# Kernel tuning notes

Hardware: AMD Instinct MI355X
Metric: run time of the kernel (lower is better)

## Reference

```python
import jax, jax.numpy as jnp
import numpy as np

N, M = 4096, 8192
IN_DIM, OUT_DIM = 4096, 1024
NUM_SAMPLE = 10


def setup_inputs() -> dict:
    key = jax.random.key(0)
    k1, k2, k3, k4, k5 = jax.random.split(key, 5)
    node_features = jax.random.normal(k1, (N, IN_DIM), dtype=jnp.float32)
    neighbor_features = jax.random.normal(k2, (M, IN_DIM), dtype=jnp.float32)
    # Xavier-ish scale for params
    weight = jax.random.normal(k3, (OUT_DIM, IN_DIM), dtype=jnp.float32) * (1.0 / np.sqrt(IN_DIM))
    attention_vector = jax.random.normal(k4, (2 * OUT_DIM, 1), dtype=jnp.float32) * 0.05
    neighbor_idx = jax.random.randint(k5, (N, NUM_SAMPLE), 0, M, dtype=jnp.int32)
    return {
        "node_features": node_features,
        "neighbor_features": neighbor_features,
        "weight": weight,
        "attention_vector": attention_vector,
        "neighbor_idx": neighbor_idx,
    }


def reference(node_features, neighbor_features, weight, attention_vector, neighbor_idx):
    # Linear transform: [N, out], [M, out]
    node_t = node_features @ weight.T
    neigh_t = neighbor_features @ weight.T

    # combined @ attention_vector decomposes:
    # cat([h_i, h_j]) @ a == h_i @ a1 + h_j @ a2  (same math, no [N,M,2*out] tensor)
    a1 = attention_vector[:OUT_DIM, 0]   # [out]
    a2 = attention_vector[OUT_DIM:, 0]   # [out]
    scores = jax.nn.leaky_relu((node_t @ a1)[:, None] + (neigh_t @ a2)[None, :],
                               negative_slope=0.2)  # [N, M]

    # Build dense 0/1 mask from sampled neighbor indices (ragged -> dense)
    rows = jnp.arange(N, dtype=jnp.int32)[:, None]                  # [N,1]
    mask = jnp.zeros((N, M), dtype=jnp.float32).at[rows, neighbor_idx].set(1.0)

    scores = jnp.where(mask == 0, -jnp.inf, scores)
    attn = jax.nn.softmax(scores, axis=1)           # masked softmax over neighbor pool
    return attn @ neigh_t                           # [N, out]
```

## Files before the change

kernel.cpp:

```cpp
#include <hip/hip_runtime.h>

#define IN_DIM  4096
#define OUT_DIM 1024
#define NN      4096
#define MM      8192
#define NSAMP   10

typedef __bf16 bf16x8 __attribute__((ext_vector_type(8)));
typedef float  fx4    __attribute__((ext_vector_type(4)));

__device__ __forceinline__ ushort f2bf(float f) {
    union { float f; unsigned u; } v; v.f = f;
    unsigned u = v.u;
    return (ushort)((u + 0x7FFFu + ((u >> 16) & 1u)) >> 16);
}
__device__ __forceinline__ float bf2f(ushort u) {
    union { unsigned u; float f; } v; v.u = ((unsigned)u) << 16;
    return v.f;
}

#define GLDS(g, l) __builtin_amdgcn_global_load_lds(                           \
    (const __attribute__((address_space(1))) unsigned*)(g),                    \
    (__attribute__((address_space(3))) unsigned*)(l), 16, 0, 0)

__global__ __launch_bounds__(256) void k_attvec(const float* __restrict__ W,
                                                const float* __restrict__ att,
                                                float* __restrict__ v1,
                                                float* __restrict__ v2,
                                                ushort* __restrict__ Wbf) {
    int k  = blockIdx.x * 256 + threadIdx.x;
    int o0 = blockIdx.y * 16;
    float s1 = 0.f, s2 = 0.f;
#pragma unroll
    for (int o = o0; o < o0 + 16; ++o) {
        float w = W[(size_t)o * IN_DIM + k];
        Wbf[(size_t)o * IN_DIM + k] = f2bf(w);
        s1 += att[o] * w;
        s2 += att[OUT_DIM + o] * w;
    }
    atomicAdd(&v1[k], s1);
    atomicAdd(&v2[k], s2);
}

__global__ __launch_bounds__(256) void k_rows(const float* __restrict__ node_f,
                                              const float* __restrict__ neigh_f,
                                              const float* __restrict__ v1,
                                              const float* __restrict__ v2,
                                              float* __restrict__ nalpha,
                                              float* __restrict__ nbeta,
                                              ushort* __restrict__ Abf) {
    int row  = blockIdx.x * 4 + (threadIdx.x >> 6);
    int lane = threadIdx.x & 63;
    float s = 0.f;
    if (row < NN) {
        const float4* xr = reinterpret_cast<const float4*>(node_f + (size_t)row * IN_DIM);
        const float4* vr = reinterpret_cast<const float4*>(v1);
#pragma unroll 1
        for (int it = 0; it < 4; ++it) {
            int base = lane + it * 256;
            float4 a0 = xr[base], a1 = xr[base + 64], a2 = xr[base + 128], a3 = xr[base + 192];
            float4 b0 = vr[base], b1 = vr[base + 64], b2 = vr[base + 128], b3 = vr[base + 192];
            s += a0.x * b0.x + a0.y * b0.y + a0.z * b0.z + a0.w * b0.w;
            s += a1.x * b1.x + a1.y * b1.y + a1.z * b1.z + a1.w * b1.w;
            s += a2.x * b2.x + a2.y * b2.y + a2.z * b2.z + a2.w * b2.w;
            s += a3.x * b3.x + a3.y * b3.y + a3.z * b3.z + a3.w * b3.w;
        }
    } else {
        int j = row - NN;
        const float4* xr = reinterpret_cast<const float4*>(neigh_f + (size_t)j * IN_DIM);
        const float4* vr = reinterpret_cast<const float4*>(v2);
        ushort4* yr = reinterpret_cast<ushort4*>(Abf + (size_t)j * IN_DIM);
#pragma unroll 1
        for (int it = 0; it < 4; ++it) {
            int base = lane + it * 256;
            float4 a0 = xr[base], a1 = xr[base + 64], a2 = xr[base + 128], a3 = xr[base + 192];
            float4 b0 = vr[base], b1 = vr[base + 64], b2 = vr[base + 128], b3 = vr[base + 192];
            s += a0.x * b0.x + a0.y * b0.y + a0.z * b0.z + a0.w * b0.w;
            s += a1.x * b1.x + a1.y * b1.y + a1.z * b1.z + a1.w * b1.w;
            s += a2.x * b2.x + a2.y * b2.y + a2.z * b2.z + a2.w * b2.w;
            s += a3.x * b3.x + a3.y * b3.y + a3.z * b3.z + a3.w * b3.w;
            ushort4 o0, o1, o2, o3;
            o0.x = f2bf(a0.x); o0.y = f2bf(a0.y); o0.z = f2bf(a0.z); o0.w = f2bf(a0.w);
            o1.x = f2bf(a1.x); o1.y = f2bf(a1.y); o1.z = f2bf(a1.z); o1.w = f2bf(a1.w);
            o2.x = f2bf(a2.x); o2.y = f2bf(a2.y); o2.z = f2bf(a2.z); o2.w = f2bf(a2.w);
            o3.x = f2bf(a3.x); o3.y = f2bf(a3.y); o3.z = f2bf(a3.z); o3.w = f2bf(a3.w);
            yr[base]       = o0;
            yr[base + 64]  = o1;
            yr[base + 128] = o2;
            yr[base + 192] = o3;
        }
    }
#pragma unroll
    for (int off = 32; off > 0; off >>= 1) s += __shfl_down(s, off, 64);
    if (lane == 0) {
        if (row < NN) nalpha[row] = s; else nbeta[row - NN] = s;
    }
}

#define TM 128
#define TN 128
#define BK 64
#define KSPLIT (IN_DIM / 2)

__global__ __launch_bounds__(256, 4) void k_gemm(const ushort* __restrict__ A,
                                                 const ushort* __restrict__ B,
                                                 ushort* __restrict__ P) {
    __shared__ __align__(16) ushort As[TM * BK];
    __shared__ __align__(16) ushort Bs[TN * BK];
    const int tid  = threadIdx.x;
    const int lane = tid & 63;
    const int wave = tid >> 6;
    const int wm   = (wave >> 1) * 64;
    const int wn   = (wave & 1) * 64;
    const int lrow = lane & 15;
    const int q    = lane >> 4;

    const int bm  = blockIdx.x * TM;
    const int bn  = blockIdx.y * TN;
    const int bz  = blockIdx.z;
    const int kb  = bz * KSPLIT;

    const int sr  = wave * 32 + (lane >> 3);
    const int sco = (((lane & 7) ^ (lane >> 3)) << 3);
    const ushort* gA = A + (size_t)(bm + sr) * IN_DIM + kb + sco;
    const ushort* gB = B + (size_t)(bn + sr) * IN_DIM + kb + sco;
    ushort* lA = As + wave * 2048;
    ushort* lB = Bs + wave * 2048;

    const int c0u = ((q ^ (lrow & 7)) << 3);

    fx4 acc[4][4] = {};

    for (int k0 = 0; k0 < KSPLIT; k0 += BK) {
#pragma unroll
        for (int i = 0; i < 4; ++i)
            GLDS(gA + k0 + (size_t)i * 8 * IN_DIM, lA + i * 512);
#pragma unroll
        for (int i = 0; i < 4; ++i)
            GLDS(gB + k0 + (size_t)i * 8 * IN_DIM, lB + i * 512);
        __syncthreads();

#pragma unroll
        for (int s = 0; s < 2; ++s) {
            const int co = c0u ^ (s << 5);
            bf16x8 af[4], bfr[4];
#pragma unroll
            for (int mi = 0; mi < 4; ++mi)
                af[mi] = *reinterpret_cast<const bf16x8*>(As + (wm + mi * 16 + lrow) * BK + co);
#pragma unroll
            for (int ni = 0; ni < 4; ++ni)
                bfr[ni] = *reinterpret_cast<const bf16x8*>(Bs + (wn + ni * 16 + lrow) * BK + co);
#pragma unroll
            for (int mi = 0; mi < 4; ++mi)
#pragma unroll
                for (int ni = 0; ni < 4; ++ni)
                    acc[mi][ni] = __builtin_amdgcn_mfma_f32_16x16x32_bf16(af[mi], bfr[ni], acc[mi][ni], 0, 0, 0);
        }
        __syncthreads();
    }

    ushort* Pz = P + (size_t)bz * MM * OUT_DIM;
#pragma unroll
    for (int mi = 0; mi < 4; ++mi)
#pragma unroll
        for (int ni = 0; ni < 4; ++ni) {
            int r = bm + wm + mi * 16 + q * 4;
            int c = bn + wn + ni * 16 + lrow;
#pragma unroll
            for (int v = 0; v < 4; ++v)
                Pz[(size_t)(r + v) * OUT_DIM + c] = f2bf(acc[mi][ni][v]);
        }
}

__global__ __launch_bounds__(256) void k_aggregate(const ushort* __restrict__ P,
                                                   const float* __restrict__ nalpha,
                                                   const float* __restrict__ nbeta,
                                                   const int* __restrict__ nidx,
                                                   float* __restrict__ outp) {
    int row = blockIdx.x;
    __shared__ int   s_idx[NSAMP];
    __shared__ float s_w[NSAMP];
    if (threadIdx.x < 16) {
        int t = threadIdx.x;
        int j = (t < NSAMP) ? nidx[row * NSAMP + t] : -1;
        float score = -INFINITY;
        if (t < NSAMP) {
            float x = nalpha[row] + nbeta[j];
            score = x > 0.f ? x : 0.2f * x;
        }
        bool dup = false;
#pragma unroll
        for (int sIdx = 0; sIdx < NSAMP; ++sIdx) {
            int js = __shfl(j, sIdx, 16);
            if (sIdx < t && js == j) dup = true;
        }
        float mx = score;
#pragma unroll
        for (int off = 8; off > 0; off >>= 1) {
            float o = __shfl_xor(mx, off, 16);
            mx = o > mx ? o : mx;
        }
        float e = (t < NSAMP && !dup) ? expf(score - mx) : 0.f;
        float sum = e;
#pragma unroll
        for (int off = 8; off > 0; off >>= 1) sum += __shfl_xor(sum, off, 16);
        if (t < NSAMP) {
            s_idx[t] = j;
            s_w[t]   = e / sum;
        }
    }
    __syncthreads();
    int col = threadIdx.x * 4;
    const ushort* P1 = P + (size_t)MM * OUT_DIM;
    float ax = 0.f, ay = 0.f, az = 0.f, aw = 0.f;
#pragma unroll
    for (int b = 0; b < 2; ++b) {
        ushort4 u0[5], u1[5];
        float   w[5];
#pragma unroll
        for (int t = 0; t < 5; ++t) {
            size_t off = (size_t)s_idx[b * 5 + t] * OUT_DIM + col;
            u0[t] = *reinterpret_cast<const ushort4*>(P + off);
            u1[t] = *reinterpret_cast<const ushort4*>(P1 + off);
            w[t]  = s_w[b * 5 + t];
        }
#pragma unroll
        for (int t = 0; t < 5; ++t) {
            ax += w[t] * (bf2f(u0[t].x) + bf2f(u1[t].x));
            ay += w[t] * (bf2f(u0[t].y) + bf2f(u1[t].y));
            az += w[t] * (bf2f(u0[t].z) + bf2f(u1[t].z));
            aw += w[t] * (bf2f(u0[t].w) + bf2f(u1[t].w));
        }
    }
    float4 o; o.x = ax; o.y = ay; o.z = az; o.w = aw;
    *reinterpret_cast<float4*>(outp + (size_t)row * OUT_DIM + col) = o;
}

extern "C" void kernel_launch(void* const* d_in, const int* in_sizes, int n_in,
                              void* d_out, int out_size, void* d_ws, size_t ws_size,
                              hipStream_t stream) {
    const float* node_f  = (const float*)d_in[0];
    const float* neigh_f = (const float*)d_in[1];
    const float* W       = (const float*)d_in[2];
    const float* att     = (const float*)d_in[3];
    const int*   nidx    = (const int*)d_in[4];
    float* outp = (float*)d_out;

    char* ws = (char*)d_ws;
    ushort* Abf = (ushort*)ws;
    ushort* Wbf = (ushort*)(ws + 67108864);
    ushort* P   = (ushort*)(ws + 75497472);
    float*  v1     = (float*)(ws + 109051904);
    float*  v2     = v1 + IN_DIM;
    float*  nalpha = v2 + IN_DIM;
    float*  nbeta  = nalpha + NN;

    hipMemsetAsync(v1, 0, 2 * IN_DIM * sizeof(float), stream);

    k_attvec   <<<dim3(16, 64),   256, 0, stream>>>(W, att, v1, v2, Wbf);
    k_rows     <<<(NN + MM) / 4,  256, 0, stream>>>(node_f, neigh_f, v1, v2, nalpha, nbeta, Abf);
    k_gemm     <<<dim3(64, 8, 2), 256, 0, stream>>>(Abf, Wbf, P);
    k_aggregate<<<NN,             256, 0, stream>>>(P, nalpha, nbeta, nidx, outp);
}
```

Baseline: 369.1 us.

## Fuse neighbor bf16 conversion and beta dot product into GEMM A-tile load

The separate pass that converted neighbor_features to bf16 and wrote it to workspace is removed. The GEMM now streams fp32 neighbor rows straight into LDS, converts them to bf16 in registers, and, for blocks with blockIdx.y==0, also computes the nbeta dot products with v2 and accumulates them atomically. This saves a 128MB read plus a 64MB write and reread of the bf16 copy. In exchange, the GEMM's A-side traffic and LDS footprint double per K step, BK shrinks to 32 (more barriers), and the y==0 blocks carry extra work, so load is uneven across blocks.

```diff
diff --git a/kernel.cpp b/kernel.cpp
--- a/kernel.cpp
+++ b/kernel.cpp
@@ -42,71 +42,42 @@
     atomicAdd(&v2[k], s2);
 }
 
-__global__ __launch_bounds__(256) void k_rows(const float* __restrict__ node_f,
-                                              const float* __restrict__ neigh_f,
-                                              const float* __restrict__ v1,
-                                              const float* __restrict__ v2,
-                                              float* __restrict__ nalpha,
-                                              float* __restrict__ nbeta,
-                                              ushort* __restrict__ Abf) {
+__global__ __launch_bounds__(256) void k_rows_node(const float* __restrict__ node_f,
+                                                   const float* __restrict__ v1,
+                                                   float* __restrict__ nalpha) {
     int row  = blockIdx.x * 4 + (threadIdx.x >> 6);
     int lane = threadIdx.x & 63;
+    const float4* xr = reinterpret_cast<const float4*>(node_f + (size_t)row * IN_DIM);
+    const float4* vr = reinterpret_cast<const float4*>(v1);
     float s = 0.f;
-    if (row < NN) {
-        const float4* xr = reinterpret_cast<const float4*>(node_f + (size_t)row * IN_DIM);
-        const float4* vr = reinterpret_cast<const float4*>(v1);
 #pragma unroll 1
-        for (int it = 0; it < 4; ++it) {
-            int base = lane + it * 256;
-            float4 a0 = xr[base], a1 = xr[base + 64], a2 = xr[base + 128], a3 = xr[base + 192];
-            float4 b0 = vr[base], b1 = vr[base + 64], b2 = vr[base + 128], b3 = vr[base + 192];
-            s += a0.x * b0.x + a0.y * b0.y + a0.z * b0.z + a0.w * b0.w;
-            s += a1.x * b1.x + a1.y * b1.y + a1.z * b1.z + a1.w * b1.w;
-            s += a2.x * b2.x + a2.y * b2.y + a2.z * b2.z + a2.w * b2.w;
-            s += a3.x * b3.x + a3.y * b3.y + a3.z * b3.z + a3.w * b3.w;
-        }
-    } else {
-        int j = row - NN;
-        const float4* xr = reinterpret_cast<const float4*>(neigh_f + (size_t)j * IN_DIM);
-        const float4* vr = reinterpret_cast<const float4*>(v2);
-        ushort4* yr = reinterpret_cast<ushort4*>(Abf + (size_t)j * IN_DIM);
-#pragma unroll 1
-        for (int it = 0; it < 4; ++it) {
-            int base = lane + it * 256;
-            float4 a0 = xr[base], a1 = xr[base + 64], a2 = xr[base + 128], a3 = xr[base + 192];
-            float4 b0 = vr[base], b1 = vr[base + 64], b2 = vr[base + 128], b3 = vr[base + 192];
-            s += a0.x * b0.x + a0.y * b0.y + a0.z * b0.z + a0.w * b0.w;
-            s += a1.x * b1.x + a1.y * b1.y + a1.z * b1.z + a1.w * b1.w;
-            s += a2.x * b2.x + a2.y * b2.y + a2.z * b2.z + a2.w * b2.w;
-            s += a3.x * b3.x + a3.y * b3.y + a3.z * b3.z + a3.w * b3.w;
-            ushort4 o0, o1, o2, o3;
-            o0.x = f2bf(a0.x); o0.y = f2bf(a0.y); o0.z = f2bf(a0.z); o0.w = f2bf(a0.w);
-            o1.x = f2bf(a1.x); o1.y = f2bf(a1.y); o1.z = f2bf(a1.z); o1.w = f2bf(a1.w);
-            o2.x = f2bf(a2.x); o2.y = f2bf(a2.y); o2.z = f2bf(a2.z); o2.w = f2bf(a2.w);
-            o3.x = f2bf(a3.x); o3.y = f2bf(a3.y); o3.z = f2bf(a3.z); o3.w = f2bf(a3.w);
-            yr[base]       = o0;
-            yr[base + 64]  = o1;
-            yr[base + 128] = o2;
-            yr[base + 192] = o3;
-        }
+    for (int it = 0; it < 4; ++it) {
+        int base = lane + it * 256;
+        float4 a0 = xr[base], a1 = xr[base + 64], a2 = xr[base + 128], a3 = xr[base + 192];
+        float4 b0 = vr[base], b1 = vr[base + 64], b2 = vr[base + 128], b3 = vr[base + 192];
+        s += a0.x * b0.x + a0.y * b0.y + a0.z * b0.z + a0.w * b0.w;
+        s += a1.x * b1.x + a1.y * b1.y + a1.z * b1.z + a1.w * b1.w;
+        s += a2.x * b2.x + a2.y * b2.y + a2.z * b2.z + a2.w * b2.w;
+        s += a3.x * b3.x + a3.y * b3.y + a3.z * b3.z + a3.w * b3.w;
     }
 #pragma unroll
     for (int off = 32; off > 0; off >>= 1) s += __shfl_down(s, off, 64);
-    if (lane == 0) {
-        if (row < NN) nalpha[row] = s; else nbeta[row - NN] = s;
-    }
+    if (lane == 0) nalpha[row] = s;
 }
 
 #define TM 128
 #define TN 128
-#define BK 64
+#define BKR 32
 #define KSPLIT (IN_DIM / 2)
 
-__global__ __launch_bounds__(256, 4) void k_gemm(const ushort* __restrict__ A,
+__global__ __launch_bounds__(256, 4) void k_gemm(const float* __restrict__ Af,
                                                  const ushort* __restrict__ B,
-                                                 ushort* __restrict__ P) {
-    __shared__ __align__(16) ushort As[TM * BK];
-    __shared__ __align__(16) ushort Bs[TN * BK];
+                                                 ushort* __restrict__ P,
+                                                 const float* __restrict__ v2,
+                                                 float* __restrict__ nbeta) {
+    __shared__ __align__(16) float  Asf[TM * BKR];
+    __shared__ __align__(16) ushort Bs[TN * BKR];
+    __shared__ __align__(16) float  v2s[KSPLIT];
     const int tid  = threadIdx.x;
     const int lane = tid & 63;
     const int wave = tid >> 6;
@@ -119,44 +90,78 @@
     const int bn  = blockIdx.y * TN;
     const int bz  = blockIdx.z;
     const int kb  = bz * KSPLIT;
-
-    const int sr  = wave * 32 + (lane >> 3);
-    const int sco = (((lane & 7) ^ (lane >> 3)) << 3);
-    const ushort* gA = A + (size_t)(bm + sr) * IN_DIM + kb + sco;
-    const ushort* gB = B + (size_t)(bn + sr) * IN_DIM + kb + sco;
-    ushort* lA = As + wave * 2048;
-    ushort* lB = Bs + wave * 2048;
-
-    const int c0u = ((q ^ (lrow & 7)) << 3);
+    const bool dofuse = (blockIdx.y == 0);
+
+    const int srA = tid >> 3;
+    const int scA = (((tid & 7) ^ (srA & 7)) << 2);
+    const float* gA = Af + (size_t)(bm + srA) * IN_DIM + kb + scA;
+
+    const int srB = tid >> 2;
+    const int scB = (((tid & 3) ^ (srB & 3)) << 3);
+    const ushort* gB = B + (size_t)(bn + srB) * IN_DIM + kb + scB;
+
+    if (dofuse) {
+#pragma unroll
+        for (int i = 0; i < 2; ++i)
+            *reinterpret_cast<float4*>(&v2s[tid * 8 + i * 4]) =
+                *reinterpret_cast<const float4*>(&v2[kb + tid * 8 + i * 4]);
+    }
+
+    const int r2 = tid >> 1;
+    const int h2 = tid & 1;
+    float sdot = 0.f;
 
     fx4 acc[4][4] = {};
 
-    for (int k0 = 0; k0 < KSPLIT; k0 += BK) {
+    for (int k0 = 0; k0 < KSPLIT; k0 += BKR) {
 #pragma unroll
         for (int i = 0; i < 4; ++i)
-            GLDS(gA + k0 + (size_t)i * 8 * IN_DIM, lA + i * 512);
-#pragma unroll
-        for (int i = 0; i < 4; ++i)
-            GLDS(gB + k0 + (size_t)i * 8 * IN_DIM, lB + i * 512);
+            GLDS(gA + k0 + (size_t)i * 32 * IN_DIM,
+                 Asf + i * 1024 + wave * 256);
+#pragma unroll
+        for (int i = 0; i < 2; ++i)
+            GLDS(gB + k0 + (size_t)i * 64 * IN_DIM,
+                 Bs + i * 2048 + wave * 512);
         __syncthreads();
 
-#pragma unroll
-        for (int s = 0; s < 2; ++s) {
-            const int co = c0u ^ (s << 5);
-            bf16x8 af[4], bfr[4];
-#pragma unroll
-            for (int mi = 0; mi < 4; ++mi)
-                af[mi] = *reinterpret_cast<const bf16x8*>(As + (wm + mi * 16 + lrow) * BK + co);
+        bf16x8 af[4], bfr[4];
+#pragma unroll
+        for (int mi = 0; mi < 4; ++mi) {
+            const int row  = wm + mi * 16 + lrow;
+            const int base = row * BKR;
+            fx4 f0 = *reinterpret_cast<const fx4*>(&Asf[base + (((2 * q)     ^ (lrow & 7)) << 2)]);
+            fx4 f1 = *reinterpret_cast<const fx4*>(&Asf[base + (((2 * q + 1) ^ (lrow & 7)) << 2)]);
+            bf16x8 t;
+            t[0] = (__bf16)f0[0]; t[1] = (__bf16)f0[1]; t[2] = (__bf16)f0[2]; t[3] = (__bf16)f0[3];
+            t[4] = (__bf16)f1[0]; t[5] = (__bf16)f1[1]; t[6] = (__bf16)f1[2]; t[7] = (__bf16)f1[3];
+            af[mi] = t;
+        }
+#pragma unroll
+        for (int ni = 0; ni < 4; ++ni) {
+            const int row = wn + ni * 16 + lrow;
+            bfr[ni] = *reinterpret_cast<const bf16x8*>(&Bs[row * BKR + ((q ^ (lrow & 3)) << 3)]);
+        }
+
+        if (dofuse) {
+#pragma unroll
+            for (int c = 0; c < 4; ++c) {
+                fx4 a = *reinterpret_cast<const fx4*>(&Asf[r2 * BKR + (((h2 * 4 + c) ^ (r2 & 7)) << 2)]);
+                fx4 b = *reinterpret_cast<const fx4*>(&v2s[k0 + h2 * 16 + c * 4]);
+                sdot += a[0] * b[0] + a[1] * b[1] + a[2] * b[2] + a[3] * b[3];
+            }
+        }
+
+#pragma unroll
+        for (int mi = 0; mi < 4; ++mi)
 #pragma unroll
             for (int ni = 0; ni < 4; ++ni)
-                bfr[ni] = *reinterpret_cast<const bf16x8*>(Bs + (wn + ni * 16 + lrow) * BK + co);
-#pragma unroll
-            for (int mi = 0; mi < 4; ++mi)
-#pragma unroll
-                for (int ni = 0; ni < 4; ++ni)
-                    acc[mi][ni] = __builtin_amdgcn_mfma_f32_16x16x32_bf16(af[mi], bfr[ni], acc[mi][ni], 0, 0, 0);
-        }
+                acc[mi][ni] = __builtin_amdgcn_mfma_f32_16x16x32_bf16(af[mi], bfr[ni], acc[mi][ni], 0, 0, 0);
         __syncthreads();
+    }
+
+    if (dofuse) {
+        sdot += __shfl_xor(sdot, 1, 64);
+        if (h2 == 0) atomicAdd(&nbeta[bm + r2], sdot);
     }
 
     ushort* Pz = P + (size_t)bz * MM * OUT_DIM;
@@ -247,18 +252,17 @@
     float* outp = (float*)d_out;
 
     char* ws = (char*)d_ws;
-    ushort* Abf = (ushort*)ws;
-    ushort* Wbf = (ushort*)(ws + 67108864);
-    ushort* P   = (ushort*)(ws + 75497472);
-    float*  v1     = (float*)(ws + 109051904);
+    ushort* Wbf = (ushort*)ws;
+    ushort* P   = (ushort*)(ws + 8388608);
+    float*  v1     = (float*)(ws + 41943040);
     float*  v2     = v1 + IN_DIM;
-    float*  nalpha = v2 + IN_DIM;
-    float*  nbeta  = nalpha + NN;
-
-    hipMemsetAsync(v1, 0, 2 * IN_DIM * sizeof(float), stream);
+    float*  nbeta  = v2 + IN_DIM;
+    float*  nalpha = nbeta + MM;
+
+    hipMemsetAsync(v1, 0, (2 * IN_DIM + MM) * sizeof(float), stream);
 
     k_attvec   <<<dim3(16, 64),   256, 0, stream>>>(W, att, v1, v2, Wbf);
-    k_rows     <<<(NN + MM) / 4,  256, 0, stream>>>(node_f, neigh_f, v1, v2, nalpha, nbeta, Abf);
-    k_gemm     <<<dim3(64, 8, 2), 256, 0, stream>>>(Abf, Wbf, P);
+    k_gemm     <<<dim3(64, 8, 2), 256, 0, stream>>>(neigh_f, Wbf, P, v2, nbeta);
+    k_rows_node<<<NN / 4,         256, 0, stream>>>(node_f, v1, nalpha);
     k_aggregate<<<NN,             256, 0, stream>>>(P, nalpha, nbeta, nidx, outp);
 }
```

Result: slower. 586.2 us (+58.8%).
